# Kernel tuning notes

Hardware: AMD Instinct MI355X
Metric: run time of the kernel (lower is better)

Reference implementation:

```python
import jax, jax.numpy as jnp
import numpy as np

D = 1024      # model dimension
H = 16        # heads
DK = D // H   # head dim
DFF = 4096    # ffn hidden
B, S = 2, 2048
EPS = 1e-6
NEG_SLOPE = 0.01  # torch LeakyReLU default


def setup_inputs() -> dict:
    key = jax.random.key(0)
    ks = jax.random.split(key, 12)
    sd = 1.0 / np.sqrt(D)
    sf = 1.0 / np.sqrt(DFF)
    return {
        "x": jax.random.normal(ks[0], (B, S, D), dtype=jnp.float32),
        "wq": jax.random.uniform(ks[1], (D, D), jnp.float32, -sd, sd),
        "bq": jnp.zeros((D,), jnp.float32),
        "wk": jax.random.uniform(ks[2], (D, D), jnp.float32, -sd, sd),
        "bk": jnp.zeros((D,), jnp.float32),
        "wv": jax.random.uniform(ks[3], (D, D), jnp.float32, -sd, sd),
        "bv": jnp.zeros((D,), jnp.float32),
        "wo": jax.random.uniform(ks[4], (D, D), jnp.float32, -sd, sd),
        "bo": jnp.zeros((D,), jnp.float32),
        "g1": jnp.ones((D,), jnp.float32),
        "b1": jnp.zeros((D,), jnp.float32),
        "w_ff1": jax.random.uniform(ks[5], (D, DFF), jnp.float32, -sd, sd),
        "b_ff1": jnp.zeros((DFF,), jnp.float32),
        "w_ff2": jax.random.uniform(ks[6], (DFF, D), jnp.float32, -sf, sf),
        "b_ff2": jnp.zeros((D,), jnp.float32),
        "g2": jnp.ones((D,), jnp.float32),
        "b2": jnp.zeros((D,), jnp.float32),
    }


def _layernorm(x, g, b):
    mu = jnp.mean(x, axis=-1, keepdims=True)
    var = jnp.mean(jnp.square(x - mu), axis=-1, keepdims=True)
    return (x - mu) * jax.lax.rsqrt(var + EPS) * g + b


def reference(x, wq, bq, wk, bk, wv, bv, wo, bo, g1, b1,
              w_ff1, b_ff1, w_ff2, b_ff2, g2, b2):
    # Multi-head attention
    q = (x @ wq + bq).reshape(B, S, H, DK).transpose(0, 2, 1, 3)  # [B,H,S,DK]
    k = (x @ wk + bk).reshape(B, S, H, DK).transpose(0, 2, 1, 3)
    v = (x @ wv + bv).reshape(B, S, H, DK).transpose(0, 2, 1, 3)
    scores = jnp.einsum('bhqd,bhkd->bhqk', q, k) / np.sqrt(DK)
    attn = jax.nn.softmax(scores, axis=-1)
    ctx = jnp.einsum('bhqk,bhkd->bhqd', attn, v)
    ctx = ctx.transpose(0, 2, 1, 3).reshape(B, S, D)
    attn_out = ctx @ wo + bo
    # residual + LN1 (dropout = identity in eval)
    h = _layernorm(attn_out + x, g1, b1)
    # FFN with LeakyReLU
    ff = jnp.where(h @ w_ff1 + b_ff1 > 0,
                   h @ w_ff1 + b_ff1,
                   NEG_SLOPE * (h @ w_ff1 + b_ff1))
    ff = ff @ w_ff2 + b_ff2
    return _layernorm(ff + h, g2, b2)
```

## Files before the change

kernel.cpp:

```cpp
#include <hip/hip_runtime.h>
#include <math.h>

#define D_MODEL 1024
#define NHEAD   16
#define DKH     64
#define DFF_    4096
#define BB      2
#define SS      2048
#define MTOT    (BB*SS)
#define EPSLN   1e-6f
#define NEG_SLOPE 0.01f

typedef unsigned short u16;
typedef unsigned int   u32;
typedef __bf16 bf16x8 __attribute__((ext_vector_type(8)));
typedef float  f32x4  __attribute__((ext_vector_type(4)));
typedef u16    u16x4  __attribute__((ext_vector_type(4)));

__device__ __forceinline__ u16 f2bf(float f) {
    u32 u = __float_as_uint(f);
    u = (u + 0x7fffu + ((u >> 16) & 1u)) >> 16;
    return (u16)u;
}
__device__ __forceinline__ float bf2f(u16 u) {
    return __uint_as_float(((u32)u) << 16);
}

__device__ __forceinline__ void gload_lds16(const u16* g, u16* l) {
    __builtin_amdgcn_global_load_lds(
        (const __attribute__((address_space(1))) u32*)g,
        (__attribute__((address_space(3))) u32*)l,
        16, 0, 0);
}

__device__ __forceinline__ void transpose_tile(const float* __restrict__ W,
        u16* __restrict__ WT, int N, int out_stride, int out_row_off,
        float scale, int bx, int by, u16* T)
{
    const int t  = threadIdx.x;
    const int n0 = bx * 64;
    const int k0 = by * 64;
    #pragma unroll
    for (int i = 0; i < 4; ++i) {
        int r = i * 16 + (t >> 4);
        int c = (t & 15) * 4;
        float4 v = *(const float4*)&W[(size_t)(k0 + r) * N + n0 + c];
        T[(c + 0) * 72 + r] = f2bf(v.x * scale);
        T[(c + 1) * 72 + r] = f2bf(v.y * scale);
        T[(c + 2) * 72 + r] = f2bf(v.z * scale);
        T[(c + 3) * 72 + r] = f2bf(v.w * scale);
    }
    __syncthreads();
    #pragma unroll
    for (int i = 0; i < 4; ++i) {
        int nr = i * 16 + (t >> 4);
        int kc = (t & 15) * 4;
        u16x4 o = { T[nr*72 + kc], T[nr*72 + kc + 1], T[nr*72 + kc + 2], T[nr*72 + kc + 3] };
        *(u16x4*)&WT[(size_t)(out_row_off + n0 + nr) * out_stride + k0 + kc] = o;
    }
}

__global__ __launch_bounds__(256)
void prep(const float* __restrict__ x, u16* __restrict__ x_bf,
          const float* __restrict__ wq, const float* __restrict__ wk,
          const float* __restrict__ wv, const float* __restrict__ wo,
          const float* __restrict__ wff1, const float* __restrict__ wff2,
          u16* __restrict__ wqkvT, u16* __restrict__ woT,
          u16* __restrict__ wff1T, u16* __restrict__ wff2T,
          const float* __restrict__ bq, const float* __restrict__ bk,
          const float* __restrict__ bv, float* __restrict__ qkv_bias,
          float qscale)
{
    __shared__ u16 T[64 * 72];
    int blk = blockIdx.x;
    if (blk < 4096) {
        int i = blk * 256 + threadIdx.x;
        float4 v = ((const float4*)x)[i];
        u16x4 o = { f2bf(v.x), f2bf(v.y), f2bf(v.z), f2bf(v.w) };
        ((u16x4*)x_bf)[i] = o;
        return;
    }
    blk -= 4096;
    if (blk < 1024) {
        int which = blk >> 8, r = blk & 255;
        const float* Ws = which == 0 ? wq : which == 1 ? wk : which == 2 ? wv : wo;
        u16* Wd   = which == 3 ? woT : wqkvT;
        int off   = which == 3 ? 0 : which * 1024;
        float sc  = which == 0 ? qscale : 1.0f;
        transpose_tile(Ws, Wd, 1024, 1024, off, sc, r & 15, r >> 4, T);
        return;
    }
    blk -= 1024;
    if (blk < 1024) {
        transpose_tile(wff1, wff1T, 4096, 1024, 0, 1.0f, blk & 63, blk >> 6, T);
        return;
    }
    blk -= 1024;
    if (blk < 1024) {
        transpose_tile(wff2, wff2T, 1024, 4096, 0, 1.0f, blk & 15, blk >> 4, T);
        return;
    }
    blk -= 1024;
    int i = blk * 256 + threadIdx.x;
    qkv_bias[i] = (i < 1024) ? bq[i] * qscale
                : (i < 2048) ? bk[i - 1024] : bv[i - 2048];
}

template<int EPI>
__global__ __launch_bounds__(256)
void gemm_bf16(const u16* __restrict__ A, const u16* __restrict__ BT,
               const float* __restrict__ bias, void* __restrict__ Cout,
               u16* __restrict__ Vt, int M, int N, int k_len, int kstride)
{
    __shared__ u16 As[128 * 64];
    __shared__ u16 Bs[128 * 64];
    const int tid  = threadIdx.x;
    const int w    = tid >> 6;
    const int lane = tid & 63;
    const int lm   = lane & 15;
    const int lq   = lane >> 4;
    const int row0 = blockIdx.y * 128;
    const int col0 = blockIdx.x * 128;
    const int k_off = blockIdx.z * k_len;
    const int wrow = (w >> 1) * 64;
    const int wcol = (w & 1) * 64;

    f32x4 acc[4][4] = {};

    const int r_i = lane >> 3;
    const int csw = ((lane & 7) ^ r_i) * 8;
    const u16* a_src = A  + (size_t)(row0 + w * 32 + r_i) * kstride + k_off + csw;
    const u16* b_src = BT + (size_t)(col0 + w * 32 + r_i) * kstride + k_off + csw;
    u16* a_dst = &As[(w * 32) * 64];
    u16* b_dst = &Bs[(w * 32) * 64];

    const int fr0 = (lq ^ (lm & 7)) * 8;
    const int fr1 = ((4 + lq) ^ (lm & 7)) * 8;
    const u16* a_rd = &As[(wrow + lm) * 64];
    const u16* b_rd = &Bs[(wcol + lm) * 64];

    for (int k0 = 0; k0 < k_len; k0 += 64) {
        #pragma unroll
        for (int i = 0; i < 4; ++i) {
            gload_lds16(a_src + k0 + (size_t)(i * 8) * kstride, a_dst + (i * 8) * 64);
            gload_lds16(b_src + k0 + (size_t)(i * 8) * kstride, b_dst + (i * 8) * 64);
        }
        __syncthreads();
        #pragma unroll
        for (int h = 0; h < 2; ++h) {
            const int fo = h ? fr1 : fr0;
            bf16x8 av[4], bv[4];
            #pragma unroll
            for (int m = 0; m < 4; ++m) av[m] = *(const bf16x8*)(a_rd + m * 16 * 64 + fo);
            #pragma unroll
            for (int n = 0; n < 4; ++n) bv[n] = *(const bf16x8*)(b_rd + n * 16 * 64 + fo);
            #pragma unroll
            for (int m = 0; m < 4; ++m)
                #pragma unroll
                for (int n = 0; n < 4; ++n)
                    acc[m][n] = __builtin_amdgcn_mfma_f32_16x16x32_bf16(av[m], bv[n], acc[m][n], 0, 0, 0);
        }
        __syncthreads();
    }

    float bz[4] = {0.f, 0.f, 0.f, 0.f};
    if (EPI != 3) {
        #pragma unroll
        for (int n = 0; n < 4; ++n) bz[n] = bias[col0 + wcol + n * 16 + lm];
    }

    if (EPI == 4 && col0 >= 2048) {
        #pragma unroll
        for (int m = 0; m < 4; ++m) {
            int rbase = row0 + wrow + m * 16 + lq * 4;
            int b = rbase >> 11, s = rbase & 2047;
            #pragma unroll
            for (int n = 0; n < 4; ++n) {
                int c = col0 + wcol + n * 16 + lm - 2048;
                u16x4 pk = { f2bf(acc[m][n][0] + bz[n]), f2bf(acc[m][n][1] + bz[n]),
                             f2bf(acc[m][n][2] + bz[n]), f2bf(acc[m][n][3] + bz[n]) };
                *(u16x4*)&Vt[(size_t)((b * 16 + (c >> 6)) * 64 + (c & 63)) * 2048 + s] = pk;
            }
        }
        return;
    }

    u16* Cz = (u16*)Cout + (EPI == 3 ? (size_t)blockIdx.z * M * N : 0);
    #pragma unroll
    for (int m = 0; m < 4; ++m) {
        #pragma unroll
        for (int e = 0; e < 4; ++e) {
            int row = row0 + wrow + m * 16 + lq * 4 + e;
            #pragma unroll
            for (int n = 0; n < 4; ++n) {
                int col = col0 + wcol + n * 16 + lm;
                float v = acc[m][n][e] + bz[n];
                if (EPI == 1) v = v > 0.f ? v : NEG_SLOPE * v;
                Cz[(size_t)row * N + col] = f2bf(v);
            }
        }
    }
}

__global__ __launch_bounds__(256, 4)
void attn_mfma(const u16* __restrict__ QKV, const u16* __restrict__ Vt,
               u16* __restrict__ ctx)
{
    __shared__ u16 QP[64 * 64];
    __shared__ u16 Kb[2][64 * 64];
    __shared__ u16 Vb[2][64 * 64];
    const int tid = threadIdx.x, w = tid >> 6, lane = tid & 63;
    const int lm = lane & 15, lq = lane >> 4;
    const int q0 = blockIdx.x * 64;
    const int bh = blockIdx.y;
    const int b  = bh >> 4, h = bh & 15;
    const size_t row_b = (size_t)b * SS;
    const int ccol = h * DKH;

    const int r_i = lane >> 3;
    const int csw = ((lane & 7) ^ r_i) * 8;
    const u16* ksrc = QKV + (row_b + w * 16 + r_i) * 3072 + 1024 + ccol + csw;
    const u16* vsrc = Vt + ((size_t)bh * 64 + w * 16 + r_i) * SS + csw;
    const u16* qsrc = QKV + (row_b + q0 + w * 16 + r_i) * 3072 + ccol + csw;

    gload_lds16(qsrc,                    &QP[(w * 16) * 64]);
    gload_lds16(qsrc + (size_t)8 * 3072, &QP[(w * 16 + 8) * 64]);
    #pragma unroll
    for (int i = 0; i < 2; ++i) {
        gload_lds16(ksrc + (size_t)(i * 8) * 3072, &Kb[0][(w * 16 + i * 8) * 64]);
        gload_lds16(vsrc + (size_t)(i * 8) * SS,   &Vb[0][(w * 16 + i * 8) * 64]);
    }
    __syncthreads();

    const int fr0 = (lq ^ (lm & 7)) * 8;
    const int fr1 = ((4 + lq) ^ (lm & 7)) * 8;
    bf16x8 aq0 = *(const bf16x8*)&QP[(w * 16 + lm) * 64 + fr0];
    bf16x8 aq1 = *(const bf16x8*)&QP[(w * 16 + lm) * 64 + fr1];
    __syncthreads();

    bf16x8 ones;
    #pragma unroll
    for (int j = 0; j < 8; ++j) ones[j] = (__bf16)1.0f;

    f32x4 o[4] = {};
    f32x4 lacc = {};

    for (int kt = 0; kt < SS / 64; ++kt) {
        const int cur = kt & 1;
        if (kt < SS / 64 - 1) {
            const int nxt = cur ^ 1;
            const size_t koff = (size_t)(kt + 1) * 64;
            #pragma unroll
            for (int i = 0; i < 2; ++i) {
                gload_lds16(ksrc + (koff + i * 8) * 3072, &Kb[nxt][(w * 16 + i * 8) * 64]);
                gload_lds16(vsrc + koff + (size_t)(i * 8) * SS, &Vb[nxt][(w * 16 + i * 8) * 64]);
            }
        }
        f32x4 s[4] = {};
        #pragma unroll
        for (int n = 0; n < 4; ++n) {
            bf16x8 bk0 = *(const bf16x8*)&Kb[cur][(n * 16 + lm) * 64 + fr0];
            bf16x8 bk1 = *(const bf16x8*)&Kb[cur][(n * 16 + lm) * 64 + fr1];
            s[n] = __builtin_amdgcn_mfma_f32_16x16x32_bf16(aq0, bk0, s[n], 0, 0, 0);
            s[n] = __builtin_amdgcn_mfma_f32_16x16x32_bf16(aq1, bk1, s[n], 0, 0, 0);
        }
        const int rb = lq * 4;
        const int cw = lm & 7;
        #pragma unroll
        for (int n = 0; n < 4; ++n) {
            const int cb = n * 2 + (lm >> 3);
            #pragma unroll
            for (int e = 0; e < 4; ++e) {
                float p = __builtin_exp2f(s[n][e]);
                const int row = w * 16 + rb + e;
                QP[row * 64 + ((cb ^ ((rb + e) & 7)) * 8) + cw] =
                    (u16)((__float_as_uint(p) + 0x8000u) >> 16);
            }
        }
        bf16x8 ap0 = *(const bf16x8*)&QP[(w * 16 + lm) * 64 + fr0];
        bf16x8 ap1 = *(const bf16x8*)&QP[(w * 16 + lm) * 64 + fr1];
        #pragma unroll
        for (int n = 0; n < 4; ++n) {
            bf16x8 bv0 = *(const bf16x8*)&Vb[cur][(n * 16 + lm) * 64 + fr0];
            bf16x8 bv1 = *(const bf16x8*)&Vb[cur][(n * 16 + lm) * 64 + fr1];
            o[n] = __builtin_amdgcn_mfma_f32_16x16x32_bf16(ap0, bv0, o[n], 0, 0, 0);
            o[n] = __builtin_amdgcn_mfma_f32_16x16x32_bf16(ap1, bv1, o[n], 0, 0, 0);
        }
        lacc = __builtin_amdgcn_mfma_f32_16x16x32_bf16(ap0, ones, lacc, 0, 0, 0);
        lacc = __builtin_amdgcn_mfma_f32_16x16x32_bf16(ap1, ones, lacc, 0, 0, 0);
        __syncthreads();
    }

    #pragma unroll
    for (int e = 0; e < 4; ++e) {
        float inv = 1.0f / lacc[e];
        int row = q0 + w * 16 + lq * 4 + e;
        u16* dst = ctx + (row_b + row) * D_MODEL + ccol;
        #pragma unroll
        for (int n = 0; n < 4; ++n)
            dst[n * 16 + lm] = f2bf(o[n][e] * inv);
    }
}

template<int OUTF32, int RESBF>
__global__ __launch_bounds__(256)
void add_ln(const u16* __restrict__ C0, const u16* __restrict__ C1,
            const float* __restrict__ cbias, const void* __restrict__ resid,
            const float* __restrict__ g, const float* __restrict__ beta,
            float* __restrict__ outf, u16* __restrict__ outb)
{
    __shared__ float red[8];
    const int row = blockIdx.x;
    const int tid = threadIdx.x;
    u16x4 p0 = ((const u16x4*)(C0 + (size_t)row * D_MODEL))[tid];
    u16x4 p1 = ((const u16x4*)(C1 + (size_t)row * D_MODEL))[tid];
    float4 cb = ((const float4*)cbias)[tid];
    float4 rr;
    if (RESBF) {
        u16x4 rb = ((const u16x4*)((const u16*)resid + (size_t)row * D_MODEL))[tid];
        rr = { bf2f(rb.x), bf2f(rb.y), bf2f(rb.z), bf2f(rb.w) };
    } else {
        rr = ((const float4*)((const float*)resid + (size_t)row * D_MODEL))[tid];
    }
    float4 v = { bf2f(p0.x) + bf2f(p1.x) + cb.x + rr.x,
                 bf2f(p0.y) + bf2f(p1.y) + cb.y + rr.y,
                 bf2f(p0.z) + bf2f(p1.z) + cb.z + rr.z,
                 bf2f(p0.w) + bf2f(p1.w) + cb.w + rr.w };
    float s  = v.x + v.y + v.z + v.w;
    float sq = v.x*v.x + v.y*v.y + v.z*v.z + v.w*v.w;
    #pragma unroll
    for (int off = 32; off > 0; off >>= 1) {
        s  += __shfl_down(s,  off, 64);
        sq += __shfl_down(sq, off, 64);
    }
    const int wv = tid >> 6;
    if ((tid & 63) == 0) { red[wv] = s; red[4 + wv] = sq; }
    __syncthreads();
    float st  = red[0] + red[1] + red[2] + red[3];
    float sqt = red[4] + red[5] + red[6] + red[7];
    float mu   = st * (1.0f / D_MODEL);
    float var  = sqt * (1.0f / D_MODEL) - mu * mu;
    float rstd = rsqrtf(var + EPSLN);
    float4 gv = ((const float4*)g)[tid];
    float4 bt = ((const float4*)beta)[tid];
    float4 ov;
    ov.x = (v.x - mu) * rstd * gv.x + bt.x;
    ov.y = (v.y - mu) * rstd * gv.y + bt.y;
    ov.z = (v.z - mu) * rstd * gv.z + bt.z;
    ov.w = (v.w - mu) * rstd * gv.w + bt.w;
    if (OUTF32) {
        ((float4*)(outf + (size_t)row * D_MODEL))[tid] = ov;
    } else {
        u16x4 ob = { f2bf(ov.x), f2bf(ov.y), f2bf(ov.z), f2bf(ov.w) };
        ((u16x4*)(outb + (size_t)row * D_MODEL))[tid] = ob;
    }
}

extern "C" void kernel_launch(void* const* d_in, const int* in_sizes, int n_in,
                              void* d_out, int out_size, void* d_ws, size_t ws_size,
                              hipStream_t stream) {
    const float* x     = (const float*)d_in[0];
    const float* wq    = (const float*)d_in[1];
    const float* bq    = (const float*)d_in[2];
    const float* wk    = (const float*)d_in[3];
    const float* bk    = (const float*)d_in[4];
    const float* wv    = (const float*)d_in[5];
    const float* bv    = (const float*)d_in[6];
    const float* wo    = (const float*)d_in[7];
    const float* bo    = (const float*)d_in[8];
    const float* g1    = (const float*)d_in[9];
    const float* b1    = (const float*)d_in[10];
    const float* w_ff1 = (const float*)d_in[11];
    const float* b_ff1 = (const float*)d_in[12];
    const float* w_ff2 = (const float*)d_in[13];
    const float* b_ff2 = (const float*)d_in[14];
    const float* g2    = (const float*)d_in[15];
    const float* b2    = (const float*)d_in[16];
    float* out = (float*)d_out;

    const float qscale = 0.18033688011112042f;

    char* W = (char*)d_ws;
    u16*   x_bf    = (u16*)(W + 0);
    u16*   wqkvT   = (u16*)(W + 8388608);
    u16*   woT     = (u16*)(W + 14680064);
    u16*   wff1T   = (u16*)(W + 16777216);
    u16*   wff2T   = (u16*)(W + 25165824);
    u16*   QKV     = (u16*)(W + 33554432);
    u16*   VtG     = (u16*)(W + 58720256);
    u16*   C0      = (u16*)(W + 67108864);
    u16*   C1      = (u16*)(W + 75497472);
    u16*   h_bf    = (u16*)(W + 83886080);
    float* qkv_bias= (float*)(W + 92274688);
    u16*   ctx     = x_bf;
    u16*   ff1_bf  = QKV;

    dim3 blk(256);
    prep<<<7180, blk, 0, stream>>>(x, x_bf, wq, wk, wv, wo, w_ff1, w_ff2,
                                   wqkvT, woT, wff1T, wff2T,
                                   bq, bk, bv, qkv_bias, qscale);
    gemm_bf16<4><<<dim3(24, 32, 1), blk, 0, stream>>>(x_bf, wqkvT, qkv_bias, QKV, VtG, MTOT, 3072, 1024, 1024);
    attn_mfma<<<dim3(32, 32), blk, 0, stream>>>(QKV, VtG, ctx);
    gemm_bf16<3><<<dim3(8, 32, 2), blk, 0, stream>>>(ctx, woT, nullptr, C0, nullptr, MTOT, 1024, 512, 1024);
    add_ln<0, 0><<<MTOT, blk, 0, stream>>>(C0, C1, bo, x, g1, b1, nullptr, h_bf);
    gemm_bf16<1><<<dim3(32, 32, 1), blk, 0, stream>>>(h_bf, wff1T, b_ff1, ff1_bf, nullptr, MTOT, DFF_, 1024, 1024);
    gemm_bf16<3><<<dim3(8, 32, 2), blk, 0, stream>>>(ff1_bf, wff2T, nullptr, C0, nullptr, MTOT, 1024, 2048, 4096);
    add_ln<1, 1><<<MTOT, blk, 0, stream>>>(C0, C1, b_ff2, h_bf, g2, b2, out, nullptr);
}
```

Baseline: 347.7 us.

## Split attention waves into 2x2 query/key tiles with LDS reduction

The attention kernel previously gave each wave 16 query rows across all 64 keys of a tile. Now each wave takes 32 query rows and 32 keys (a 2x2 wave grid). K and V fragments loaded from shared memory are each reused for two query sub-tiles, which cuts LDS read traffic per MFMA. The cost is a cross-wave reduction of partial outputs and row sums through shared memory at the end, plus more accumulator registers. The shared memory used for that reduction is the K/V buffers, repurposed after the loop.

```diff
diff --git a/kernel.cpp b/kernel.cpp
--- a/kernel.cpp
+++ b/kernel.cpp
@@ -211,6 +211,8 @@
     __shared__ u16 Vb[2][64 * 64];
     const int tid = threadIdx.x, w = tid >> 6, lane = tid & 63;
     const int lm = lane & 15, lq = lane >> 4;
+    const int qh = w >> 1;
+    const int kh = w & 1;
     const int q0 = blockIdx.x * 64;
     const int bh = blockIdx.y;
     const int b  = bh >> 4, h = bh & 15;
@@ -234,16 +236,22 @@
 
     const int fr0 = (lq ^ (lm & 7)) * 8;
     const int fr1 = ((4 + lq) ^ (lm & 7)) * 8;
-    bf16x8 aq0 = *(const bf16x8*)&QP[(w * 16 + lm) * 64 + fr0];
-    bf16x8 aq1 = *(const bf16x8*)&QP[(w * 16 + lm) * 64 + fr1];
+    const int frp = kh ? fr1 : fr0;
+
+    bf16x8 aq[2][2];
+    #pragma unroll
+    for (int m = 0; m < 2; ++m) {
+        aq[m][0] = *(const bf16x8*)&QP[(qh * 32 + m * 16 + lm) * 64 + fr0];
+        aq[m][1] = *(const bf16x8*)&QP[(qh * 32 + m * 16 + lm) * 64 + fr1];
+    }
     __syncthreads();
 
     bf16x8 ones;
     #pragma unroll
     for (int j = 0; j < 8; ++j) ones[j] = (__bf16)1.0f;
 
-    f32x4 o[4] = {};
-    f32x4 lacc = {};
+    f32x4 o[2][4] = {};
+    f32x4 lacc[2] = {};
 
     for (int kt = 0; kt < SS / 64; ++kt) {
         const int cur = kt & 1;
@@ -256,49 +264,84 @@
                 gload_lds16(vsrc + koff + (size_t)(i * 8) * SS, &Vb[nxt][(w * 16 + i * 8) * 64]);
             }
         }
-        f32x4 s[4] = {};
-        #pragma unroll
-        for (int n = 0; n < 4; ++n) {
-            bf16x8 bk0 = *(const bf16x8*)&Kb[cur][(n * 16 + lm) * 64 + fr0];
-            bf16x8 bk1 = *(const bf16x8*)&Kb[cur][(n * 16 + lm) * 64 + fr1];
-            s[n] = __builtin_amdgcn_mfma_f32_16x16x32_bf16(aq0, bk0, s[n], 0, 0, 0);
-            s[n] = __builtin_amdgcn_mfma_f32_16x16x32_bf16(aq1, bk1, s[n], 0, 0, 0);
+        f32x4 s[2][2] = {};
+        #pragma unroll
+        for (int n = 0; n < 2; ++n) {
+            bf16x8 bk0 = *(const bf16x8*)&Kb[cur][(kh * 32 + n * 16 + lm) * 64 + fr0];
+            bf16x8 bk1 = *(const bf16x8*)&Kb[cur][(kh * 32 + n * 16 + lm) * 64 + fr1];
+            #pragma unroll
+            for (int m = 0; m < 2; ++m) {
+                s[m][n] = __builtin_amdgcn_mfma_f32_16x16x32_bf16(aq[m][0], bk0, s[m][n], 0, 0, 0);
+                s[m][n] = __builtin_amdgcn_mfma_f32_16x16x32_bf16(aq[m][1], bk1, s[m][n], 0, 0, 0);
+            }
         }
         const int rb = lq * 4;
         const int cw = lm & 7;
         #pragma unroll
+        for (int m = 0; m < 2; ++m) {
+            #pragma unroll
+            for (int n = 0; n < 2; ++n) {
+                const int cb = kh * 4 + n * 2 + (lm >> 3);
+                #pragma unroll
+                for (int e = 0; e < 4; ++e) {
+                    float p = __builtin_exp2f(s[m][n][e]);
+                    const int row = qh * 32 + m * 16 + rb + e;
+                    QP[row * 64 + ((cb ^ ((rb + e) & 7)) * 8) + cw] =
+                        (u16)((__float_as_uint(p) + 0x8000u) >> 16);
+                }
+            }
+        }
+        bf16x8 ap[2];
+        #pragma unroll
+        for (int m = 0; m < 2; ++m)
+            ap[m] = *(const bf16x8*)&QP[(qh * 32 + m * 16 + lm) * 64 + frp];
+        #pragma unroll
         for (int n = 0; n < 4; ++n) {
-            const int cb = n * 2 + (lm >> 3);
+            bf16x8 bv = *(const bf16x8*)&Vb[cur][(n * 16 + lm) * 64 + frp];
+            #pragma unroll
+            for (int m = 0; m < 2; ++m)
+                o[m][n] = __builtin_amdgcn_mfma_f32_16x16x32_bf16(ap[m], bv, o[m][n], 0, 0, 0);
+        }
+        #pragma unroll
+        for (int m = 0; m < 2; ++m)
+            lacc[m] = __builtin_amdgcn_mfma_f32_16x16x32_bf16(ap[m], ones, lacc[m], 0, 0, 0);
+        __syncthreads();
+    }
+
+    if (kh == 1) {
+        float* red = (float*)(qh == 0 ? (void*)Kb : (void*)Vb);
+        #pragma unroll
+        for (int m = 0; m < 2; ++m) {
+            #pragma unroll
+            for (int n = 0; n < 4; ++n)
+                #pragma unroll
+                for (int e = 0; e < 4; ++e)
+                    red[((m * 4 + n) * 4 + e) * 64 + lane] = o[m][n][e];
+            #pragma unroll
+            for (int e = 0; e < 4; ++e)
+                red[(32 + m * 4 + e) * 64 + lane] = lacc[m][e];
+        }
+    }
+    __syncthreads();
+    if (kh == 0) {
+        const float* red = (const float*)(qh == 0 ? (void*)Kb : (void*)Vb);
+        #pragma unroll
+        for (int m = 0; m < 2; ++m) {
+            #pragma unroll
+            for (int e = 0; e < 4; ++e)
+                lacc[m][e] += red[(32 + m * 4 + e) * 64 + lane];
             #pragma unroll
             for (int e = 0; e < 4; ++e) {
-                float p = __builtin_exp2f(s[n][e]);
-                const int row = w * 16 + rb + e;
-                QP[row * 64 + ((cb ^ ((rb + e) & 7)) * 8) + cw] =
-                    (u16)((__float_as_uint(p) + 0x8000u) >> 16);
-            }
-        }
-        bf16x8 ap0 = *(const bf16x8*)&QP[(w * 16 + lm) * 64 + fr0];
-        bf16x8 ap1 = *(const bf16x8*)&QP[(w * 16 + lm) * 64 + fr1];
-        #pragma unroll
-        for (int n = 0; n < 4; ++n) {
-            bf16x8 bv0 = *(const bf16x8*)&Vb[cur][(n * 16 + lm) * 64 + fr0];
-            bf16x8 bv1 = *(const bf16x8*)&Vb[cur][(n * 16 + lm) * 64 + fr1];
-            o[n] = __builtin_amdgcn_mfma_f32_16x16x32_bf16(ap0, bv0, o[n], 0, 0, 0);
-            o[n] = __builtin_amdgcn_mfma_f32_16x16x32_bf16(ap1, bv1, o[n], 0, 0, 0);
-        }
-        lacc = __builtin_amdgcn_mfma_f32_16x16x32_bf16(ap0, ones, lacc, 0, 0, 0);
-        lacc = __builtin_amdgcn_mfma_f32_16x16x32_bf16(ap1, ones, lacc, 0, 0, 0);
-        __syncthreads();
-    }
-
-    #pragma unroll
-    for (int e = 0; e < 4; ++e) {
-        float inv = 1.0f / lacc[e];
-        int row = q0 + w * 16 + lq * 4 + e;
-        u16* dst = ctx + (row_b + row) * D_MODEL + ccol;
-        #pragma unroll
-        for (int n = 0; n < 4; ++n)
-            dst[n * 16 + lm] = f2bf(o[n][e] * inv);
+                float inv = 1.0f / lacc[m][e];
+                int row = q0 + qh * 32 + m * 16 + lq * 4 + e;
+                u16* dst = ctx + (row_b + row) * D_MODEL + ccol;
+                #pragma unroll
+                for (int n = 0; n < 4; ++n) {
+                    float v = o[m][n][e] + red[((m * 4 + n) * 4 + e) * 64 + lane];
+                    dst[n * 16 + lm] = f2bf(v * inv);
+                }
+            }
+        }
     }
 }
 
```

Result: slower. 357.9 us (+2.9%).
